# Kernel optimization log

Hardware: AMD Instinct MI355X
Metric: run time of the kernel (lower is better)

Reference implementation:

```python
import jax, jax.numpy as jnp
import numpy as np

B, L, D = 8, 2048, 1024
NH, M = 32, 16            # TTTConfig defaults: num_attention_heads=32, mini_batch_size=16
HD = D // NH              # 32
NM = L // M               # 128 mini-batches
DI = 2048                 # FFN hidden (configs.d_lower)
BASE_LR = 1.0
EPS = 1e-6


def setup_inputs() -> dict:
    key = jax.random.key(0)
    ks = jax.random.split(key, 12)
    n = lambda k, s, sc=0.02: jax.random.normal(k, s, jnp.float32) * sc
    return dict(
        enc_input=jax.random.normal(ks[0], (B, L, D), jnp.float32),
        ln0_g=jnp.ones((D,), jnp.float32), ln0_b=jnp.zeros((D,), jnp.float32),
        Wq=n(ks[1], (D, D)), Wk=n(ks[2], (D, D)), Wv=n(ks[3], (D, D)), Wo=n(ks[4], (D, D)),
        W1=n(ks[5], (NH, HD, HD)), b1=jnp.zeros((NH, 1, HD), jnp.float32),
        token_idx_delta=jnp.zeros((M,), jnp.float32),
        lr_w=n(ks[6], (NH, D)), lr_b=jnp.zeros((NH,), jnp.float32),
        ttt_ln_g=jnp.ones((NH, HD), jnp.float32), ttt_ln_b=jnp.zeros((NH, HD), jnp.float32),
        post_g=jnp.ones((D,), jnp.float32), post_b=jnp.zeros((D,), jnp.float32),
        ffn_g=jnp.ones((D,), jnp.float32), ffn_b=jnp.zeros((D,), jnp.float32),
        fw1=n(ks[7], (D, DI)), fb1=jnp.zeros((DI,), jnp.float32),
        fw2=n(ks[8], (DI, D)), fb2=jnp.zeros((D,), jnp.float32),
    )


def _layernorm(x, g, b):
    mu = x.mean(-1, keepdims=True)
    v = ((x - mu) ** 2).mean(-1, keepdims=True)
    return (x - mu) * jax.lax.rsqrt(v + EPS) * g + b


def _rope(x):
    # x: [B,NH,L,HD]; standard rotary embedding, theta=10000
    half = HD // 2
    inv = 1.0 / (10000.0 ** (jnp.arange(0, HD, 2, dtype=jnp.float32) / HD))
    pos = jnp.arange(L, dtype=jnp.float32)
    fr = pos[:, None] * inv[None, :]                    # [L, HD/2]
    emb = jnp.concatenate([fr, fr], -1)                 # [L, HD]
    cos, sin = jnp.cos(emb), jnp.sin(emb)
    rot = jnp.concatenate([-x[..., half:], x[..., :half]], -1)
    return x * cos + rot * sin


def reference(enc_input, ln0_g, ln0_b, Wq, Wk, Wv, Wo, W1, b1, token_idx_delta,
              lr_w, lr_b, ttt_ln_g, ttt_ln_b, post_g, post_b,
              ffn_g, ffn_b, fw1, fb1, fw2, fb2):
    residual = enc_input
    x = _layernorm(enc_input, ln0_g, ln0_b)

    def heads(t):  # [B,L,D] -> [B,NH,L,HD]
        return t.reshape(B, L, NH, HD).transpose(0, 2, 1, 3)

    XQ = _rope(heads(x @ Wq))
    XK = _rope(heads(x @ Wk))
    XV = heads(x @ Wv)

    # per-token learnable learning rates (sigmoid gate), token_idx schedule
    X_mb = x.reshape(B, NM, M, D)
    ttt_lr = jax.nn.sigmoid(jnp.einsum('bnkc,hc->bhnk', X_mb, lr_w) + lr_b[None, :, None, None])
    ttt_lr_eta = BASE_LR * ttt_lr / HD                               # [B,NH,NM,M]
    token_idx = jnp.clip(1.0 / jnp.arange(1, M + 1, dtype=jnp.float32) + token_idx_delta, 0.0, None)
    eta = token_idx[None, None, None, :, None] * ttt_lr_eta[:, :, :, None, :]  # [B,NH,NM,M,M]

    def to_scan(t):  # [B,NH,L,HD] -> [NM,B,NH,M,HD]
        return t.reshape(B, NH, NM, M, HD).transpose(2, 0, 1, 3, 4)

    xs = (to_scan(XQ), to_scan(XK), to_scan(XV), eta.transpose(2, 0, 1, 3, 4))

    lw = ttt_ln_g[:, None, :]   # [NH,1,HD]
    lb = ttt_ln_b[:, None, :]
    tril = jnp.tril(jnp.ones((M, M), jnp.float32))

    def ln_fwd(z):
        mu = z.mean(-1, keepdims=True)
        v = ((z - mu) ** 2).mean(-1, keepdims=True)
        return (z - mu) * jax.lax.rsqrt(v + EPS) * lw + lb

    def ln_l2_bwd(z, tgt):
        # gradient of 0.5*||LN(z)-tgt||^2 w.r.t. z (fused LN l2 backward)
        mu = z.mean(-1, keepdims=True)
        v = ((z - mu) ** 2).mean(-1, keepdims=True)
        std = jnp.sqrt(v + EPS)
        xhat = (z - mu) / std
        gxh = (xhat * lw + lb - tgt) * lw
        return (HD * gxh - gxh.sum(-1, keepdims=True)
                - xhat * (gxh * xhat).sum(-1, keepdims=True)) / (HD * std)

    W1_0 = jnp.broadcast_to(W1[None], (B, NH, HD, HD))
    b1_0 = jnp.broadcast_to(b1[None], (B, NH, 1, HD))

    def step(carry, inp):
        W, bvec = carry
        q, k, v_, e = inp                                    # [B,NH,M,HD], e: [B,NH,M,M]
        Z1 = k @ W + bvec
        grad = ln_l2_bwd(Z1, v_ - k)                         # [B,NH,M,HD]
        Attn1 = tril * (q @ k.transpose(0, 1, 3, 2))         # causal dual-form attention
        b_bar = bvec - (tril * e) @ grad
        Z1_bar = q @ W - (e * Attn1) @ grad + b_bar
        last_e = e[:, :, -1, :, None]                        # [B,NH,M,1]
        W_new = W - (last_e * k).transpose(0, 1, 3, 2) @ grad
        b_new = bvec - (last_e * grad).sum(-2, keepdims=True)
        return (W_new, b_new), q + ln_fwd(Z1_bar)

    _, outs = jax.lax.scan(step, (W1_0, b1_0), xs)           # [NM,B,NH,M,HD]
    out = outs.transpose(1, 0, 3, 2, 4).reshape(B, L, D)     # -> [B,L,D]
    out = _layernorm(out, post_g, post_b) @ Wo               # post_norm + o_proj
    out = out + residual                                     # dropout = identity (eval)

    # PositionWiseFeedForward (pre-LN, residual)
    r2 = out
    h = _layernorm(out, ffn_g, ffn_b)
    h = jax.nn.relu(h @ fw1 + fb1) @ fw2 + fb2
    return h + r2
```

## Files before the change

### kernel.cpp

```cpp
#include <hip/hip_runtime.h>
#include <hip/hip_bf16.h>
#include <stdint.h>

#define B_   8
#define L_   2048
#define D_   1024
#define NH_  32
#define M_   16
#define NM_  128
#define HD_  32
#define DI_  2048
#define BL_  16384
#define EPS_ 1e-6f

typedef __attribute__((ext_vector_type(8))) short  s16x8;
typedef __attribute__((ext_vector_type(4))) short  s16x4;
typedef __attribute__((ext_vector_type(8))) __bf16 bf16x8;
typedef __attribute__((ext_vector_type(4))) float  f32x4;
typedef __attribute__((ext_vector_type(4))) unsigned u32x4;
typedef __attribute__((ext_vector_type(2))) unsigned u32x2;

__device__ __forceinline__ float bf2f(short s){
  unsigned u = ((unsigned)(unsigned short)s) << 16;
  return __builtin_bit_cast(float, u);
}
__device__ __forceinline__ short f2bf(float f){
  unsigned u = __builtin_bit_cast(unsigned, f);
  u = u + 0x7FFFu + ((u >> 16) & 1u);
  return (short)(u >> 16);
}
__device__ __forceinline__ unsigned cvtpk(float lo, float hi){
  unsigned r;
  asm("v_cvt_pk_bf16_f32 %0, %1, %2" : "=v"(r) : "v"(lo), "v"(hi));
  return r;
}
__device__ __forceinline__ void mfma16x2(s16x4 a, s16x4 b0, s16x4 b1,
                                         f32x4& c0, f32x4& c1){
  asm volatile(
      "s_nop 1\n\t"
      "v_mfma_f32_16x16x16_bf16 %0, %2, %3, %0\n\t"
      "v_mfma_f32_16x16x16_bf16 %1, %2, %4, %1\n\t"
      "s_nop 7\n\t"
      "s_nop 3"
      : "+v"(c0), "+v"(c1) : "v"(a), "v"(b0), "v"(b1));
}
template<int N>
__device__ __forceinline__ float ror_add(float v){
  const int y = __builtin_amdgcn_update_dpp(
      0, __builtin_bit_cast(int, v), 0x120 + N, 0xF, 0xF, true);
  return v + __builtin_bit_cast(float, y);
}
__device__ __forceinline__ float rsum16d(float v){
  v = ror_add<1>(v); v = ror_add<2>(v); v = ror_add<4>(v); v = ror_add<8>(v);
  return v;
}
__device__ __forceinline__ void wgbar(){
  asm volatile("s_waitcnt lgkmcnt(0)" ::: "memory");
  __builtin_amdgcn_s_barrier();
  __builtin_amdgcn_sched_barrier(0);
}
__device__ __forceinline__ void gl16(const void* g, void* l){
  __builtin_amdgcn_global_load_lds(
      (const __attribute__((address_space(1))) void*)g,
      (__attribute__((address_space(3))) void*)l, 16, 0, 0);
}

__global__ __launch_bounds__(256) void transpose_cast(
    const float* __restrict__ in, short* __restrict__ out, int R, int Cc)
{
  __shared__ float t[32][33];
  const int lx = threadIdx.x & 31, ly = threadIdx.x >> 5;
  const int r0 = blockIdx.y * 32, c0 = blockIdx.x * 32;
  #pragma unroll
  for (int s = 0; s < 4; ++s){
    const int r = ly + s*8;
    t[r][lx] = in[(size_t)(r0 + r)*Cc + c0 + lx];
  }
  __syncthreads();
  #pragma unroll
  for (int s = 0; s < 4; ++s){
    const int r = ly + s*8;
    out[(size_t)(c0 + r)*R + r0 + lx] = f2bf(t[lx][r]);
  }
}

struct TC4 { const float *s0,*s1,*s2,*s3; short *d0,*d1,*d2,*d3; };
__global__ __launch_bounds__(256) void transpose_cast4(TC4 p)
{
  __shared__ float t[32][33];
  const int z = blockIdx.z;
  const float* in = (z==0)?p.s0:(z==1)?p.s1:(z==2)?p.s2:p.s3;
  short* out      = (z==0)?p.d0:(z==1)?p.d1:(z==2)?p.d2:p.d3;
  const int lx = threadIdx.x & 31, ly = threadIdx.x >> 5;
  const int r0 = blockIdx.y * 32, c0 = blockIdx.x * 32;
  #pragma unroll
  for (int s = 0; s < 4; ++s){
    const int r = ly + s*8;
    t[r][lx] = in[(size_t)(r0 + r)*1024 + c0 + lx];
  }
  __syncthreads();
  #pragma unroll
  for (int s = 0; s < 4; ++s){
    const int r = ly + s*8;
    out[(size_t)(c0 + r)*1024 + r0 + lx] = f2bf(t[lx][r]);
  }
}

__global__ __launch_bounds__(256) void misc_prep(
    const float* __restrict__ lr_w, short* __restrict__ lrwb,
    float* __restrict__ ct, float* __restrict__ st)
{
  const int idx = blockIdx.x*256 + threadIdx.x;
  if (idx < NH_*D_){
    lrwb[idx] = f2bf(lr_w[idx]);
  } else {
    const int k = idx - NH_*D_;
    const int l = k >> 4, j = k & 15;
    const float inv = powf(10000.f, -(float)j * (1.f/16.f));
    const float fr  = (float)l * inv;
    ct[k] = cosf(fr);
    st[k] = sinf(fr);
  }
}

__global__ __launch_bounds__(256) void ln_rows(
    const float* __restrict__ in, const float* __restrict__ g,
    const float* __restrict__ bta, short* __restrict__ out)
{
  const int row = blockIdx.x, tid = threadIdx.x;
  const float4 v = ((const float4*)(in + (size_t)row*D_))[tid];
  float s  = v.x + v.y + v.z + v.w;
  float s2 = v.x*v.x + v.y*v.y + v.z*v.z + v.w*v.w;
  #pragma unroll
  for (int m = 1; m < 64; m <<= 1){ s += __shfl_xor(s, m); s2 += __shfl_xor(s2, m); }
  __shared__ float rs[4], rq[4];
  if ((tid & 63) == 0){ rs[tid>>6] = s; rq[tid>>6] = s2; }
  __syncthreads();
  s  = rs[0] + rs[1] + rs[2] + rs[3];
  s2 = rq[0] + rq[1] + rq[2] + rq[3];
  const float mu   = s  * (1.f/D_);
  const float var  = s2 * (1.f/D_) - mu*mu;
  const float rstd = rsqrtf(var + EPS_);
  const float4 gg = ((const float4*)g)[tid];
  const float4 bb = ((const float4*)bta)[tid];
  s16x4 o;
  o[0] = f2bf((v.x - mu)*rstd*gg.x + bb.x);
  o[1] = f2bf((v.y - mu)*rstd*gg.y + bb.y);
  o[2] = f2bf((v.z - mu)*rstd*gg.z + bb.z);
  o[3] = f2bf((v.w - mu)*rstd*gg.w + bb.w);
  ((s16x4*)(out + (size_t)row*D_))[tid] = o;
}

__global__ __launch_bounds__(256) void ln_rows_bf(
    const short* __restrict__ in, const float* __restrict__ g,
    const float* __restrict__ bta, short* __restrict__ out)
{
  const int row = blockIdx.x, tid = threadIdx.x;
  const s16x4 v4 = ((const s16x4*)(in + (size_t)row*D_))[tid];
  float v[4];
  #pragma unroll
  for (int e = 0; e < 4; ++e) v[e] = bf2f(v4[e]);
  float s  = v[0]+v[1]+v[2]+v[3];
  float s2 = v[0]*v[0]+v[1]*v[1]+v[2]*v[2]+v[3]*v[3];
  #pragma unroll
  for (int m = 1; m < 64; m <<= 1){ s += __shfl_xor(s, m); s2 += __shfl_xor(s2, m); }
  __shared__ float rs[4], rq[4];
  if ((tid & 63) == 0){ rs[tid>>6] = s; rq[tid>>6] = s2; }
  __syncthreads();
  s  = rs[0] + rs[1] + rs[2] + rs[3];
  s2 = rq[0] + rq[1] + rq[2] + rq[3];
  const float mu   = s  * (1.f/D_);
  const float var  = s2 * (1.f/D_) - mu*mu;
  const float rstd = rsqrtf(var + EPS_);
  const float4 gg = ((const float4*)g)[tid];
  const float4 bb = ((const float4*)bta)[tid];
  s16x4 o;
  #pragma unroll
  for (int e = 0; e < 4; ++e){
    const float gv = (e==0)?gg.x:(e==1)?gg.y:(e==2)?gg.z:gg.w;
    const float bv = (e==0)?bb.x:(e==1)?bb.y:(e==2)?bb.z:bb.w;
    o[e] = f2bf((v[e] - mu)*rstd*gv + bv);
  }
  ((s16x4*)(out + (size_t)row*D_))[tid] = o;
}

template<int ACT, int OUTBF, int BIAS, int RES, int RESB, int QKVOUT>
__global__ __launch_bounds__(512, 2) void gemm256(
    const short* __restrict__ A, const short* __restrict__ Bt,
    const float* __restrict__ bias, const float* __restrict__ res,
    const short* __restrict__ resb,
    float* __restrict__ Cf, short* __restrict__ Cb,
    const float* __restrict__ ct, const float* __restrict__ st,
    int Mr, int N, int K)
{
  __shared__ __align__(16) short As[4][8192];
  __shared__ __align__(16) short Bs[4][8192];
  const int tid  = threadIdx.x;
  const int lane = tid & 63, wid = tid >> 6;
  const int wr = wid >> 2, wc = wid & 3;
  const int nwg = gridDim.x * gridDim.y;
  const int wg  = blockIdx.y * gridDim.x + blockIdx.x;
  const int swz = (wg & 7) * (nwg >> 3) + (wg >> 3);
  const int bx  = swz % gridDim.x, by = swz / gridDim.x;
  const int row0 = by * 256, col0 = bx * 256;

  f32x4 acc[8][4] = {};

  const int kswz = (((tid & 3) ^ ((tid >> 3) & 3)) << 3);
  const short* gAb = A  + (size_t)(row0 + (tid >> 2)) * K + kswz;
  const short* gBb = Bt + (size_t)(col0 + (tid >> 2)) * K + kswz;
  short* lAb = &As[0][0] + tid*8;
  short* lBb = &Bs[0][0] + tid*8;

  auto stage = [&](int bt2, int t2){
    const size_t kb = (size_t)t2 * 32;
    gl16(gAb + kb,                   lAb + bt2*8192);
    gl16(gAb + kb + 128*(size_t)K,   lAb + bt2*8192 + 4096);
    gl16(gBb + kb,                   lBb + bt2*8192);
    gl16(gBb + kb + 128*(size_t)K,   lBb + bt2*8192 + 4096);
  };

  const int fr = lane & 15;
  const int k0 = (((lane >> 4) ^ ((lane >> 1) & 3)) << 3);

  const int nK = K >> 5;
  stage(0, 0); stage(1, 1); stage(2, 2);
  asm volatile("s_waitcnt vmcnt(8)" ::: "memory");
  __builtin_amdgcn_s_barrier();

  for (int kt = 0; kt < nK; ++kt){
    const int bt = kt & 3;
    const short* Ab = &As[0][0] + bt*8192 + wr*4096;
    const short* Bb = &Bs[0][0] + bt*8192 + (wc >> 1)*4096 + (wc & 1)*2048;
    bf16x8 af[8], bfv[4];
    #pragma unroll
    for (int m = 0; m < 8; ++m)
      af[m] = *(const bf16x8*)(Ab + (m*16 + fr)*32 + k0);
    #pragma unroll
    for (int n = 0; n < 4; ++n)
      bfv[n] = *(const bf16x8*)(Bb + (n*16 + fr)*32 + k0);
    if (kt + 3 < nK) stage((kt + 3) & 3, kt + 3);
    __builtin_amdgcn_s_setprio(1);
    #pragma unroll
    for (int m = 0; m < 8; ++m)
      #pragma unroll
      for (int n = 0; n < 4; ++n)
        acc[m][n] = __builtin_amdgcn_mfma_f32_16x16x32_bf16(af[m], bfv[n], acc[m][n], 0,0,0);
    __builtin_amdgcn_s_setprio(0);
    if (kt + 3 < nK)      asm volatile("s_waitcnt vmcnt(8)" ::: "memory");
    else if (kt + 2 < nK) asm volatile("s_waitcnt vmcnt(4)" ::: "memory");
    else if (kt + 1 < nK) asm volatile("s_waitcnt vmcnt(0)" ::: "memory");
    __builtin_amdgcn_s_barrier();
  }

  const int cr = (lane >> 4) * 4, cc = lane & 15;
  if (QKVOUT){
    const int part = col0 >> 10;
    #pragma unroll
    for (int m = 0; m < 8; ++m){
      const int gr0 = row0 + wr*128 + m*16 + cr;
      const int bidx = gr0 >> 11, l0 = gr0 & (L_-1);
      const int nn = l0 >> 4;
      if (part < 2){
        #pragma unroll
        for (int np = 0; np < 2; ++np){
          const int gc = col0 + wc*64 + np*32 + cc;
          const int hh = (gc & 1023) >> 5;
          short* tile = Cb + ((size_t)(bidx*NH_ + hh)*NM_ + nn)*2048;
          s16x4 r0v, r1v;
          #pragma unroll
          for (int r = 0; r < 4; ++r){
            const int l = l0 + r;
            const float cv = ct[l*16 + cc], sv = st[l*16 + cc];
            const float x0 = acc[m][np*2][r], x1 = acc[m][np*2+1][r];
            const short q0 = f2bf(x0*cv - x1*sv);
            const short q1 = f2bf(x1*cv + x0*sv);
            tile[part*512 + (cr + r)*32 + cc]      = q0;
            tile[part*512 + (cr + r)*32 + cc + 16] = q1;
            r0v[r] = q0; r1v[r] = q1;
          }
          if (part == 1){
            *(s16x4*)(tile + 1024 + cc*16 + cr)      = r0v;
            *(s16x4*)(tile + 1024 + (cc+16)*16 + cr) = r1v;
          }
        }
      } else {
        #pragma unroll
        for (int n = 0; n < 4; ++n){
          const int gc = col0 + wc*64 + n*16 + cc;
          const int hh = (gc & 1023) >> 5, dd = gc & 31;
          short* tile = Cb + ((size_t)(bidx*NH_ + hh)*NM_ + nn)*2048;
          s16x4 p;
          #pragma unroll
          for (int r = 0; r < 4; ++r) p[r] = f2bf(acc[m][n][r]);
          *(s16x4*)(tile + 1536 + dd*16 + cr) = p;
        }
      }
    }
    return;
  }
  #pragma unroll
  for (int m = 0; m < 8; ++m){
    #pragma unroll
    for (int n = 0; n < 4; ++n){
      const int gc = col0 + wc*64 + n*16 + cc;
      float bv = 0.f;
      if (BIAS) bv = bias[gc];
      #pragma unroll
      for (int r = 0; r < 4; ++r){
        const int gr = row0 + wr*128 + m*16 + cr + r;
        float v = acc[m][n][r] + bv;
        if (RES)  v += res[(size_t)gr*N + gc];
        if (RESB) v += bf2f(resb[(size_t)gr*N + gc]);
        if (ACT == 1) v = fmaxf(v, 0.f);
        if (OUTBF) Cb[(size_t)gr*N + gc] = f2bf(v);
        else       Cf[(size_t)gr*N + gc] = v;
      }
    }
  }
}

__global__ __launch_bounds__(256) void eta_kernel(
    const short* __restrict__ xb, const short* __restrict__ lrwb,
    const float* __restrict__ lr_b, float* __restrict__ eta)
{
  __shared__ __align__(16) short wl[NH_*1032];
  const int tid = threadIdx.x;
  const int lane = tid & 63, wv = tid >> 6;
  const int li = lane & 15, lh = lane >> 4;
  #pragma unroll
  for (int s = 0; s < 16; ++s){
    const int e = tid + 256*s;
    const int hrow = e >> 7, c = (e & 127) * 8;
    *(s16x8*)(wl + hrow*1032 + c) = ((const s16x8*)lrwb)[e];
  }
  __syncthreads();

  const int t0 = (blockIdx.x*4 + wv) * 16;
  const short* xrow = xb + (size_t)(t0 + li)*1024 + 8*lh;
  const short* w0p = wl + li*1032 + 8*lh;
  const short* w1p = wl + (16 + li)*1032 + 8*lh;
  f32x4 acc0 = {}, acc1 = {};
  #pragma unroll 4
  for (int s = 0; s < 32; ++s){
    const bf16x8 a  = *(const bf16x8*)(xrow + s*32);
    const bf16x8 b0 = *(const bf16x8*)(w0p + s*32);
    const bf16x8 b1 = *(const bf16x8*)(w1p + s*32);
    acc0 = __builtin_amdgcn_mfma_f32_16x16x32_bf16(a, b0, acc0, 0,0,0);
    acc1 = __builtin_amdgcn_mfma_f32_16x16x32_bf16(a, b1, acc1, 0,0,0);
  }
  const int t = t0 + 4*lh;
  const int bidx = t >> 11, l = t & (L_-1), n = l >> 4, im = l & 15;
  float* e0 = eta + ((size_t)(bidx*NH_ + li)*NM_ + n)*M_ + im;
  float* e1 = eta + ((size_t)(bidx*NH_ + 16 + li)*NM_ + n)*M_ + im;
  const float lb0 = lr_b[li], lb1 = lr_b[16 + li];
  #pragma unroll
  for (int r = 0; r < 4; ++r){
    e0[r] = 1.f/(1.f + __expf(-(acc0[r] + lb0))) * (1.f/32.f);
    e1[r] = 1.f/(1.f + __expf(-(acc1[r] + lb1))) * (1.f/32.f);
  }
}

__global__ __launch_bounds__(192) void scan_kernel(
    const short* __restrict__ Q5, const float* __restrict__ eta,
    const float* __restrict__ W1, const float* __restrict__ b1,
    const float* __restrict__ tdelta, const float* __restrict__ lng,
    const float* __restrict__ lnb, short* __restrict__ out)
{
  const int bh = blockIdx.x;
  const int h = bh & 31, b = bh >> 5;
  const int lane = threadIdx.x & 63;
  const int wv = threadIdx.x >> 6;
  const int li = lane & 15, lh = lane >> 4;

  __shared__ __align__(16) short WTl[2][32*40];
  __shared__ __align__(16) unsigned PGl[2][256];
  __shared__ float BBl[2][2][16];
  __shared__ __align__(16) short QLl[2][16*40];

  const short* chain = Q5 + (size_t)bh * (NM_*2048);
  const float* ech   = eta + (size_t)bh * (NM_*16);

  float lw[2], lbv[2];
  #pragma unroll
  for (int hh = 0; hh < 2; ++hh){
    lw[hh]  = lng[h*32 + 16*hh + li];
    lbv[hh] = lnb[h*32 + 16*hh + li];
  }

  if (wv == 0){
    f32x4 Wq[2][2];
    #pragma unroll
    for (int rb = 0; rb < 2; ++rb)
      #pragma unroll
      for (int cb = 0; cb < 2; ++cb)
        #pragma unroll
        for (int r = 0; r < 4; ++r)
          Wq[rb][cb][r] = W1[h*1024 + (16*rb + 4*lh + r)*32 + 16*cb + li];
    float bb[2];
    bb[0] = b1[h*32 + li];  bb[1] = b1[h*32 + 16 + li];
    const float lef = fmaxf(1.f/16.f + tdelta[15], 0.f);

    auto writeWT = [&](int sl){
      #pragma unroll
      for (int cb = 0; cb < 2; ++cb)
        #pragma unroll
        for (int rb = 0; rb < 2; ++rb){
          const unsigned p0 = cvtpk(Wq[rb][cb][0], Wq[rb][cb][1]);
          const unsigned p1 = cvtpk(Wq[rb][cb][2], Wq[rb][cb][3]);
          *(uint64_t*)(&WTl[sl][0] + (16*cb + li)*40 + 16*rb + 4*lh) =
              ((uint64_t)p1 << 32) | p0;
        }
    };
    auto readWf = [&](int sl, bf16x8* Wf){
      Wf[0] = *(const bf16x8*)(&WTl[sl][0] + li*40 + 8*lh);
      Wf[1] = *(const bf16x8*)(&WTl[sl][0] + (16 + li)*40 + 8*lh);
    };

    writeWT(0);
    if (lh == 0){ BBl[0][0][li] = bb[0]; BBl[0][1][li] = bb[1]; }
    bf16x8 Wf[2];
    readWf(0, Wf);

    struct P0 { s16x8 kA; s16x4 kTe0, kTe1, vTe0, vTe1;
                f32x4 lr0, lr1, lr2, lr3; };
    auto ld0 = [&](int n) -> P0 {
      const short* t = chain + (size_t)n*2048;
      const float* e = ech + n*16;
      P0 p;
      p.kA   = *(const s16x8*)(t + 512 + li*32 + 8*lh);
      p.kTe0 = *(const s16x4*)(t + 1024 + li*16 + 4*lh);
      p.kTe1 = *(const s16x4*)(t + 1024 + (16 + li)*16 + 4*lh);
      p.vTe0 = *(const s16x4*)(t + 1536 + li*16 + 4*lh);
      p.vTe1 = *(const s16x4*)(t + 1536 + (16 + li)*16 + 4*lh);
      p.lr0 = *(const f32x4*)(e);     p.lr1 = *(const f32x4*)(e + 4);
      p.lr2 = *(const f32x4*)(e + 8); p.lr3 = *(const f32x4*)(e + 12);
      return p;
    };

    P0 cur = ld0(0);
    wgbar();

    #pragma unroll 1
    for (int p = 0; p <= NM_; ++p){
      if (p < NM_){
        const int n = p;
        const int sl = n & 1;
        P0 nxt = ld0(n + 1 < NM_ ? n + 1 : NM_ - 1);
        const bf16x8 kAf = __builtin_bit_cast(bf16x8, cur.kA);

        f32x4 zac[2];
        #pragma unroll
        for (int hh = 0; hh < 2; ++hh){
          f32x4 c0; c0[0]=bb[hh]; c0[1]=bb[hh]; c0[2]=bb[hh]; c0[3]=bb[hh];
          zac[hh] = __builtin_amdgcn_mfma_f32_16x16x32_bf16(kAf, Wf[hh], c0, 0,0,0);
        }

        float xh[2][4], grad[2][4], rstdv[4];
        #pragma unroll
        for (int r = 0; r < 4; ++r){
          float s  = rsum16d(zac[0][r] + zac[1][r]);
          float q2 = rsum16d(zac[0][r]*zac[0][r] + zac[1][r]*zac[1][r]);
          const float mu  = s * (1.f/32.f);
          const float var = q2 * (1.f/32.f) - mu*mu;
          const float rstd = rsqrtf(var + EPS_);
          rstdv[r] = rstd;
          xh[0][r] = (zac[0][r] - mu) * rstd;
          xh[1][r] = (zac[1][r] - mu) * rstd;
        }
        #pragma unroll
        for (int r = 0; r < 4; ++r){
          const float t0 = bf2f(cur.vTe0[r]) - bf2f(cur.kTe0[r]);
          const float t1 = bf2f(cur.vTe1[r]) - bf2f(cur.kTe1[r]);
          const float g0 = (xh[0][r]*lw[0] + lbv[0] - t0)*lw[0];
          const float g1 = (xh[1][r]*lw[1] + lbv[1] - t1)*lw[1];
          const float sg  = rsum16d(g0 + g1);
          const float sgx = rsum16d(g0*xh[0][r] + g1*xh[1][r]);
          const float f = rstdv[r] * (1.f/32.f);
          grad[0][r] = (32.f*g0 - sg - xh[0][r]*sgx) * f;
          grad[1][r] = (32.f*g1 - sg - xh[1][r]*sgx) * f;
        }

        const unsigned g00 = cvtpk(grad[0][0], grad[0][1]);
        const unsigned g01 = cvtpk(grad[0][2], grad[0][3]);
        const unsigned g10 = cvtpk(grad[1][0], grad[1][1]);
        const unsigned g11 = cvtpk(grad[1][2], grad[1][3]);
        u32x4 gq; gq[0]=g00; gq[1]=g01; gq[2]=g10; gq[3]=g11;
        *(u32x4*)&PGl[sl][lane*4] = gq;
        u32x2 tg0; tg0[0]=g00; tg0[1]=g01;
        u32x2 tg1; tg1[0]=g10; tg1[1]=g11;
        const s16x4 gB0 = __builtin_bit_cast(s16x4, tg0);
        const s16x4 gB1 = __builtin_bit_cast(s16x4, tg1);

        f32x4 lrq;
        { const f32x4 t0 = (lh & 1) ? cur.lr1 : cur.lr0;
          const f32x4 t1 = (lh & 1) ? cur.lr3 : cur.lr2;
          lrq = (lh & 2) ? t1 : t0; }

        #pragma unroll
        for (int rb = 0; rb < 2; ++rb){
          const s16x4 kq = rb ? cur.kTe1 : cur.kTe0;
          const unsigned a0 = cvtpk(-lef*lrq[0]*bf2f(kq[0]), -lef*lrq[1]*bf2f(kq[1]));
          const unsigned a1 = cvtpk(-lef*lrq[2]*bf2f(kq[2]), -lef*lrq[3]*bf2f(kq[3]));
          u32x2 ta; ta[0]=a0; ta[1]=a1;
          const s16x4 afq = __builtin_bit_cast(s16x4, ta);
          mfma16x2(afq, gB0, gB1, Wq[rb][0], Wq[rb][1]);
        }

        writeWT(sl ^ 1);
        readWf(sl ^ 1, Wf);

        #pragma unroll
        for (int hh = 0; hh < 2; ++hh){
          float t = 0.f;
          #pragma unroll
          for (int r = 0; r < 4; ++r) t += lrq[r]*grad[hh][r];
          t += __shfl_xor(t, 16); t += __shfl_xor(t, 32);
          bb[hh] -= lef * t;
        }
        if (lh == 0){ BBl[sl ^ 1][0][li] = bb[0]; BBl[sl ^ 1][1][li] = bb[1]; }
        cur = nxt;
      }
      wgbar();
    }
  } else {
    const int par = wv - 1;
    const float tok_i = fmaxf(1.f/(float)(li+1) + tdelta[li], 0.f);
    short* outp = out + (size_t)b*L_*D_ + h*32;

    struct P1 { s16x8 qA, kA; f32x4 lr0, lr1, lr2, lr3; };
    auto ld1 = [&](int n) -> P1 {
      const short* t = chain + (size_t)n*2048;
      const float* e = ech + n*16;
      P1 p;
      p.qA = *(const s16x8*)(t + li*32 + 8*lh);
      p.kA = *(const s16x8*)(t + 512 + li*32 + 8*lh);
      p.lr0 = *(const f32x4*)(e);     p.lr1 = *(const f32x4*)(e + 4);
      p.lr2 = *(const f32x4*)(e + 8); p.lr3 = *(const f32x4*)(e + 12);
      return p;
    };

    auto outln = [&](int n, const f32x4* yac){
      #pragma unroll
      for (int r = 0; r < 4; ++r){
        const float s  = rsum16d(yac[0][r] + yac[1][r]);
        const float q2 = rsum16d(yac[0][r]*yac[0][r] + yac[1][r]*yac[1][r]);
        const float mu   = s * (1.f/32.f);
        const float var  = q2 * (1.f/32.f) - mu*mu;
        const float rstd = rsqrtf(var + EPS_);
        const int row = 4*lh + r;
        #pragma unroll
        for (int hh = 0; hh < 2; ++hh){
          const float qv = bf2f(QLl[n & 1][row*40 + 16*hh + li]);
          const float o  = qv + (yac[hh][r] - mu)*rstd*lw[hh] + lbv[hh];
          outp[(size_t)(n*16 + row)*D_ + 16*hh + li] = f2bf(o);
        }
      }
    };

    P1 cur = ld1(par);
    wgbar();

    f32x4 ycur[2] = {};
    s16x4 pCur4 = {};
    #pragma unroll 1
    for (int p = 0; p <= NM_; ++p){
      if (p >= 1 && ((p - 1) & 1) == par){
        const int m = p - 1;
        const int sl = m & 1;
        const u32x4 gq = *(const u32x4*)&PGl[sl][lane*4];
        u32x2 tg0; tg0[0]=gq[0]; tg0[1]=gq[1];
        u32x2 tg1; tg1[0]=gq[2]; tg1[1]=gq[3];
        const s16x4 gB0 = __builtin_bit_cast(s16x4, tg0);
        const s16x4 gB1 = __builtin_bit_cast(s16x4, tg1);
        mfma16x2(pCur4, gB0, gB1, ycur[0], ycur[1]);
        outln(m, ycur);
      }
      if (p < NM_ && (p & 1) == par){
        const int sl = p & 1;
        bf16x8 Wf0 = *(const bf16x8*)(&WTl[sl][0] + li*40 + 8*lh);
        bf16x8 Wf1 = *(const bf16x8*)(&WTl[sl][0] + (16 + li)*40 + 8*lh);
        const float bb0 = BBl[sl][0][li];
        const float bb1 = BBl[sl][1][li];

        P1 nxt = ld1(p + 2 < NM_ ? p + 2 : p);
        const bf16x8 qAf = __builtin_bit_cast(bf16x8, cur.qA);
        const bf16x8 kAf = __builtin_bit_cast(bf16x8, cur.kA);

        *(s16x8*)(&QLl[sl][0] + li*40 + 8*lh) = cur.qA;

        f32x4 zz = {};
        const f32x4 aacT = __builtin_amdgcn_mfma_f32_16x16x32_bf16(kAf, qAf, zz, 0,0,0);

        f32x4 lrq;
        { const f32x4 t0 = (lh & 1) ? cur.lr1 : cur.lr0;
          const f32x4 t1 = (lh & 1) ? cur.lr3 : cur.lr2;
          lrq = (lh & 2) ? t1 : t0; }

        float pv[4];
        #pragma unroll
        for (int e = 0; e < 4; ++e){
          const bool ok = (4*lh + e <= li);
          pv[e] = ok ? -tok_i * lrq[e] * (1.f + aacT[e]) : 0.f;
        }
        u32x2 tp; tp[0] = cvtpk(pv[0], pv[1]); tp[1] = cvtpk(pv[2], pv[3]);
        pCur4 = __builtin_bit_cast(s16x4, tp);

        { f32x4 c0; c0[0]=bb0; c0[1]=bb0; c0[2]=bb0; c0[3]=bb0;
          ycur[0] = __builtin_amdgcn_mfma_f32_16x16x32_bf16(qAf, Wf0, c0, 0,0,0); }
        { f32x4 c0; c0[0]=bb1; c0[1]=bb1; c0[2]=bb1; c0[3]=bb1;
          ycur[1] = __builtin_amdgcn_mfma_f32_16x16x32_bf16(qAf, Wf1, c0, 0,0,0); }

        cur = nxt;
      }
      wgbar();
    }
  }
}

extern "C" void kernel_launch(void* const* d_in, const int* in_sizes, int n_in,
                              void* d_out, int out_size, void* d_ws, size_t ws_size,
                              hipStream_t stream)
{
  const float* enc    = (const float*)d_in[0];
  const float* ln0_g  = (const float*)d_in[1];
  const float* ln0_b  = (const float*)d_in[2];
  const float* Wq     = (const float*)d_in[3];
  const float* Wk     = (const float*)d_in[4];
  const float* Wv     = (const float*)d_in[5];
  const float* Wo     = (const float*)d_in[6];
  const float* W1     = (const float*)d_in[7];
  const float* b1     = (const float*)d_in[8];
  const float* tdelta = (const float*)d_in[9];
  const float* lr_w   = (const float*)d_in[10];
  const float* lr_b   = (const float*)d_in[11];
  const float* ttt_g  = (const float*)d_in[12];
  const float* ttt_b  = (const float*)d_in[13];
  const float* post_g = (const float*)d_in[14];
  const float* post_b = (const float*)d_in[15];
  const float* ffn_g  = (const float*)d_in[16];
  const float* ffn_b  = (const float*)d_in[17];
  const float* fw1    = (const float*)d_in[18];
  const float* fb1    = (const float*)d_in[19];
  const float* fw2    = (const float*)d_in[20];
  const float* fb2    = (const float*)d_in[21];

  char* ws = (char*)d_ws;
  short* Q5    = (short*)(ws + 0);
  short* XB    = (short*)(ws + 134217728);
  short* SCANB = (short*)(ws + 134217728);
  short* WQKVT = (short*)(ws + 167772160);
  short* WOT   = (short*)(ws + 174063616);
  short* FW1T  = (short*)(ws + 176160768);
  short* FW2T  = (short*)(ws + 180355072);
  short* LRWB  = (short*)(ws + 184549376);
  float* CT    = (float*)(ws + 184614912);
  float* ST    = (float*)(ws + 184745984);
  float* ETA   = (float*)(ws + 184877056);
  short* YB    = (short*)(ws + 0);
  short* HB    = (short*)(ws + 33554432);
  short* T1    = (short*)(ws + 67108864);
  short* R2B   = (short*)(ws + 134217728);
  float* R2    = (float*)d_out;

  dim3 b256(256), b512(512);
  TC4 tc;
  tc.s0 = Wq; tc.s1 = Wk; tc.s2 = Wv; tc.s3 = Wo;
  tc.d0 = WQKVT; tc.d1 = WQKVT + 1048576; tc.d2 = WQKVT + 2097152; tc.d3 = WOT;
  transpose_cast4<<<dim3(32,32,4), b256, 0, stream>>>(tc);
  transpose_cast<<<dim3(64,32), b256, 0, stream>>>(fw1, FW1T, D_, DI_);
  transpose_cast<<<dim3(32,64), b256, 0, stream>>>(fw2, FW2T, DI_, D_);
  misc_prep<<<dim3(256), b256, 0, stream>>>(lr_w, LRWB, CT, ST);

  ln_rows<<<BL_, b256, 0, stream>>>(enc, ln0_g, ln0_b, XB);
  gemm256<0,0,0,0,0,1><<<dim3(12,64), b512, 0, stream>>>(XB, WQKVT, nullptr, nullptr, nullptr,
                                                         nullptr, Q5, CT, ST, BL_, 3072, D_);
  eta_kernel<<<dim3(256), b256, 0, stream>>>(XB, LRWB, lr_b, ETA);
  scan_kernel<<<dim3(256), dim3(192), 0, stream>>>(Q5, ETA, W1, b1, tdelta,
                                                   ttt_g, ttt_b, SCANB);
  ln_rows_bf<<<BL_, b256, 0, stream>>>(SCANB, post_g, post_b, YB);
  gemm256<0,1,0,1,0,0><<<dim3(4,64), b512, 0, stream>>>(YB, WOT, nullptr, enc, nullptr,
                                                        nullptr, R2B, nullptr, nullptr, BL_, D_, D_);
  ln_rows_bf<<<BL_, b256, 0, stream>>>(R2B, ffn_g, ffn_b, HB);
  gemm256<1,1,1,0,0,0><<<dim3(8,64), b512, 0, stream>>>(HB, FW1T, fb1, nullptr, nullptr,
                                                        nullptr, T1, nullptr, nullptr, BL_, DI_, D_);
  gemm256<0,0,1,0,1,0><<<dim3(4,64), b512, 0, stream>>>(T1, FW2T, fb2, nullptr, R2B,
                                                        R2, nullptr, nullptr, nullptr, BL_, D_, DI_);
}
```

Measured before the change: 507.9 us.

## Process two mini-batches per barrier in scan and deepen LDS ring to eight slots

The producer wave now runs two sequential mini-batch updates per workgroup barrier, with a two-deep register prefetch of chain data. Shared buffers for W, gradients and bias grow from two to eight slots so it can run ahead. The two consumer waves each handle one mini-batch per superstep, lagging by one superstep. Each consumer now does its attention, gradient MFMA and output layernorm in one step instead of splitting them across barriers. The aim is to halve the barrier count on the serial recurrence, at the cost of more LDS and register pressure.

Measured after the change: 485.1 us (median of 2 runs). -4.5%, faster.

```diff
diff --git a/kernel.cpp b/kernel.cpp
--- a/kernel.cpp
+++ b/kernel.cpp
@@ -373,9 +373,9 @@
   const int wv = threadIdx.x >> 6;
   const int li = lane & 15, lh = lane >> 4;
 
-  __shared__ __align__(16) short WTl[2][32*40];
-  __shared__ __align__(16) unsigned PGl[2][256];
-  __shared__ float BBl[2][2][16];
+  __shared__ __align__(16) short WTl[8][32*40];
+  __shared__ __align__(16) unsigned PGl[8][256];
+  __shared__ float BBl[8][2][16];
   __shared__ __align__(16) short QLl[2][16*40];
 
   const short* chain = Q5 + (size_t)bh * (NM_*2048);
@@ -439,87 +439,92 @@
     };
 
     P0 cur = ld0(0);
+    P0 nxt = ld0(1);
     wgbar();
 
     #pragma unroll 1
-    for (int p = 0; p <= NM_; ++p){
-      if (p < NM_){
-        const int n = p;
-        const int sl = n & 1;
-        P0 nxt = ld0(n + 1 < NM_ ? n + 1 : NM_ - 1);
-        const bf16x8 kAf = __builtin_bit_cast(bf16x8, cur.kA);
-
-        f32x4 zac[2];
+    for (int p = 0; p <= 64; ++p){
+      if (p < 64){
         #pragma unroll
-        for (int hh = 0; hh < 2; ++hh){
-          f32x4 c0; c0[0]=bb[hh]; c0[1]=bb[hh]; c0[2]=bb[hh]; c0[3]=bb[hh];
-          zac[hh] = __builtin_amdgcn_mfma_f32_16x16x32_bf16(kAf, Wf[hh], c0, 0,0,0);
+        for (int s = 0; s < 2; ++s){
+          const int n = 2*p + s;
+          P0 pf = ld0(n + 2 < NM_ ? n + 2 : NM_ - 1);
+          const bf16x8 kAf = __builtin_bit_cast(bf16x8, cur.kA);
+
+          f32x4 zac[2];
+          #pragma unroll
+          for (int hh = 0; hh < 2; ++hh){
+            f32x4 c0; c0[0]=bb[hh]; c0[1]=bb[hh]; c0[2]=bb[hh]; c0[3]=bb[hh];
+            zac[hh] = __builtin_amdgcn_mfma_f32_16x16x32_bf16(kAf, Wf[hh], c0, 0,0,0);
+          }
+
+          float xh[2][4], grad[2][4], rstdv[4];
+          #pragma unroll
+          for (int r = 0; r < 4; ++r){
+            float ss = rsum16d(zac[0][r] + zac[1][r]);
+            float q2 = rsum16d(zac[0][r]*zac[0][r] + zac[1][r]*zac[1][r]);
+            const float mu  = ss * (1.f/32.f);
+            const float var = q2 * (1.f/32.f) - mu*mu;
+            const float rstd = rsqrtf(var + EPS_);
+            rstdv[r] = rstd;
+            xh[0][r] = (zac[0][r] - mu) * rstd;
+            xh[1][r] = (zac[1][r] - mu) * rstd;
+          }
+          #pragma unroll
+          for (int r = 0; r < 4; ++r){
+            const float t0 = bf2f(cur.vTe0[r]) - bf2f(cur.kTe0[r]);
+            const float t1 = bf2f(cur.vTe1[r]) - bf2f(cur.kTe1[r]);
+            const float g0 = (xh[0][r]*lw[0] + lbv[0] - t0)*lw[0];
+            const float g1 = (xh[1][r]*lw[1] + lbv[1] - t1)*lw[1];
+            const float sg  = rsum16d(g0 + g1);
+            const float sgx = rsum16d(g0*xh[0][r] + g1*xh[1][r]);
+            const float f = rstdv[r] * (1.f/32.f);
+            grad[0][r] = (32.f*g0 - sg - xh[0][r]*sgx) * f;
+            grad[1][r] = (32.f*g1 - sg - xh[1][r]*sgx) * f;
+          }
+
+          f32x4 lrq;
+          { const f32x4 t0 = (lh & 1) ? cur.lr1 : cur.lr0;
+            const f32x4 t1 = (lh & 1) ? cur.lr3 : cur.lr2;
+            lrq = (lh & 2) ? t1 : t0; }
+
+          float tb0 = 0.f, tb1 = 0.f;
+          #pragma unroll
+          for (int r = 0; r < 4; ++r){ tb0 += lrq[r]*grad[0][r]; tb1 += lrq[r]*grad[1][r]; }
+          tb0 += __shfl_xor(tb0, 16); tb1 += __shfl_xor(tb1, 16);
+          tb0 += __shfl_xor(tb0, 32); tb1 += __shfl_xor(tb1, 32);
+
+          const unsigned g00 = cvtpk(grad[0][0], grad[0][1]);
+          const unsigned g01 = cvtpk(grad[0][2], grad[0][3]);
+          const unsigned g10 = cvtpk(grad[1][0], grad[1][1]);
+          const unsigned g11 = cvtpk(grad[1][2], grad[1][3]);
+          u32x4 gq; gq[0]=g00; gq[1]=g01; gq[2]=g10; gq[3]=g11;
+          *(u32x4*)&PGl[n & 7][lane*4] = gq;
+          u32x2 tg0; tg0[0]=g00; tg0[1]=g01;
+          u32x2 tg1; tg1[0]=g10; tg1[1]=g11;
+          const s16x4 gB0 = __builtin_bit_cast(s16x4, tg0);
+          const s16x4 gB1 = __builtin_bit_cast(s16x4, tg1);
+
+          #pragma unroll
+          for (int rb = 0; rb < 2; ++rb){
+            const s16x4 kq = rb ? cur.kTe1 : cur.kTe0;
+            const unsigned a0 = cvtpk(-lef*lrq[0]*bf2f(kq[0]), -lef*lrq[1]*bf2f(kq[1]));
+            const unsigned a1 = cvtpk(-lef*lrq[2]*bf2f(kq[2]), -lef*lrq[3]*bf2f(kq[3]));
+            u32x2 ta; ta[0]=a0; ta[1]=a1;
+            const s16x4 afq = __builtin_bit_cast(s16x4, ta);
+            mfma16x2(afq, gB0, gB1, Wq[rb][0], Wq[rb][1]);
+          }
+
+          bb[0] -= lef * tb0;
+          bb[1] -= lef * tb1;
+
+          const int so = (n + 1) & 7;
+          writeWT(so);
+          readWf(so, Wf);
+          if (lh == 0){ BBl[so][0][li] = bb[0]; BBl[so][1][li] = bb[1]; }
+          cur = nxt;
+          nxt = pf;
         }
-
-        float xh[2][4], grad[2][4], rstdv[4];
-        #pragma unroll
-        for (int r = 0; r < 4; ++r){
-          float s  = rsum16d(zac[0][r] + zac[1][r]);
-          float q2 = rsum16d(zac[0][r]*zac[0][r] + zac[1][r]*zac[1][r]);
-          const float mu  = s * (1.f/32.f);
-          const float var = q2 * (1.f/32.f) - mu*mu;
-          const float rstd = rsqrtf(var + EPS_);
-          rstdv[r] = rstd;
-          xh[0][r] = (zac[0][r] - mu) * rstd;
-          xh[1][r] = (zac[1][r] - mu) * rstd;
-        }
-        #pragma unroll
-        for (int r = 0; r < 4; ++r){
-          const float t0 = bf2f(cur.vTe0[r]) - bf2f(cur.kTe0[r]);
-          const float t1 = bf2f(cur.vTe1[r]) - bf2f(cur.kTe1[r]);
-          const float g0 = (xh[0][r]*lw[0] + lbv[0] - t0)*lw[0];
-          const float g1 = (xh[1][r]*lw[1] + lbv[1] - t1)*lw[1];
-          const float sg  = rsum16d(g0 + g1);
-          const float sgx = rsum16d(g0*xh[0][r] + g1*xh[1][r]);
-          const float f = rstdv[r] * (1.f/32.f);
-          grad[0][r] = (32.f*g0 - sg - xh[0][r]*sgx) * f;
-          grad[1][r] = (32.f*g1 - sg - xh[1][r]*sgx) * f;
-        }
-
-        const unsigned g00 = cvtpk(grad[0][0], grad[0][1]);
-        const unsigned g01 = cvtpk(grad[0][2], grad[0][3]);
-        const unsigned g10 = cvtpk(grad[1][0], grad[1][1]);
-        const unsigned g11 = cvtpk(grad[1][2], grad[1][3]);
-        u32x4 gq; gq[0]=g00; gq[1]=g01; gq[2]=g10; gq[3]=g11;
-        *(u32x4*)&PGl[sl][lane*4] = gq;
-        u32x2 tg0; tg0[0]=g00; tg0[1]=g01;
-        u32x2 tg1; tg1[0]=g10; tg1[1]=g11;
-        const s16x4 gB0 = __builtin_bit_cast(s16x4, tg0);
-        const s16x4 gB1 = __builtin_bit_cast(s16x4, tg1);
-
-        f32x4 lrq;
-        { const f32x4 t0 = (lh & 1) ? cur.lr1 : cur.lr0;
-          const f32x4 t1 = (lh & 1) ? cur.lr3 : cur.lr2;
-          lrq = (lh & 2) ? t1 : t0; }
-
-        #pragma unroll
-        for (int rb = 0; rb < 2; ++rb){
-          const s16x4 kq = rb ? cur.kTe1 : cur.kTe0;
-          const unsigned a0 = cvtpk(-lef*lrq[0]*bf2f(kq[0]), -lef*lrq[1]*bf2f(kq[1]));
-          const unsigned a1 = cvtpk(-lef*lrq[2]*bf2f(kq[2]), -lef*lrq[3]*bf2f(kq[3]));
-          u32x2 ta; ta[0]=a0; ta[1]=a1;
-          const s16x4 afq = __builtin_bit_cast(s16x4, ta);
-          mfma16x2(afq, gB0, gB1, Wq[rb][0], Wq[rb][1]);
-        }
-
-        writeWT(sl ^ 1);
-        readWf(sl ^ 1, Wf);
-
-        #pragma unroll
-        for (int hh = 0; hh < 2; ++hh){
-          float t = 0.f;
-          #pragma unroll
-          for (int r = 0; r < 4; ++r) t += lrq[r]*grad[hh][r];
-          t += __shfl_xor(t, 16); t += __shfl_xor(t, 32);
-          bb[hh] -= lef * t;
-        }
-        if (lh == 0){ BBl[sl ^ 1][0][li] = bb[0]; BBl[sl ^ 1][1][li] = bb[1]; }
-        cur = nxt;
       }
       wgbar();
     }
@@ -540,54 +545,25 @@
       return p;
     };
 
-    auto outln = [&](int n, const f32x4* yac){
-      #pragma unroll
-      for (int r = 0; r < 4; ++r){
-        const float s  = rsum16d(yac[0][r] + yac[1][r]);
-        const float q2 = rsum16d(yac[0][r]*yac[0][r] + yac[1][r]*yac[1][r]);
-        const float mu   = s * (1.f/32.f);
-        const float var  = q2 * (1.f/32.f) - mu*mu;
-        const float rstd = rsqrtf(var + EPS_);
-        const int row = 4*lh + r;
-        #pragma unroll
-        for (int hh = 0; hh < 2; ++hh){
-          const float qv = bf2f(QLl[n & 1][row*40 + 16*hh + li]);
-          const float o  = qv + (yac[hh][r] - mu)*rstd*lw[hh] + lbv[hh];
-          outp[(size_t)(n*16 + row)*D_ + 16*hh + li] = f2bf(o);
-        }
-      }
-    };
-
     P1 cur = ld1(par);
     wgbar();
 
-    f32x4 ycur[2] = {};
-    s16x4 pCur4 = {};
     #pragma unroll 1
-    for (int p = 0; p <= NM_; ++p){
-      if (p >= 1 && ((p - 1) & 1) == par){
-        const int m = p - 1;
-        const int sl = m & 1;
-        const u32x4 gq = *(const u32x4*)&PGl[sl][lane*4];
-        u32x2 tg0; tg0[0]=gq[0]; tg0[1]=gq[1];
-        u32x2 tg1; tg1[0]=gq[2]; tg1[1]=gq[3];
-        const s16x4 gB0 = __builtin_bit_cast(s16x4, tg0);
-        const s16x4 gB1 = __builtin_bit_cast(s16x4, tg1);
-        mfma16x2(pCur4, gB0, gB1, ycur[0], ycur[1]);
-        outln(m, ycur);
-      }
-      if (p < NM_ && (p & 1) == par){
-        const int sl = p & 1;
+    for (int p = 1; p <= 65; ++p){
+      if (p >= 2){
+        const int n = 2*(p - 2) + par;
+        const int sl = n & 7;
+        P1 pf = ld1(n + 2 < NM_ ? n + 2 : NM_ - 1);
+
         bf16x8 Wf0 = *(const bf16x8*)(&WTl[sl][0] + li*40 + 8*lh);
         bf16x8 Wf1 = *(const bf16x8*)(&WTl[sl][0] + (16 + li)*40 + 8*lh);
         const float bb0 = BBl[sl][0][li];
         const float bb1 = BBl[sl][1][li];
 
-        P1 nxt = ld1(p + 2 < NM_ ? p + 2 : p);
         const bf16x8 qAf = __builtin_bit_cast(bf16x8, cur.qA);
         const bf16x8 kAf = __builtin_bit_cast(bf16x8, cur.kA);
 
-        *(s16x8*)(&QLl[sl][0] + li*40 + 8*lh) = cur.qA;
+        *(s16x8*)(&QLl[par][0] + li*40 + 8*lh) = cur.qA;
 
         f32x4 zz = {};
         const f32x4 aacT = __builtin_amdgcn_mfma_f32_16x16x32_bf16(kAf, qAf, zz, 0,0,0);
@@ -604,14 +580,37 @@
           pv[e] = ok ? -tok_i * lrq[e] * (1.f + aacT[e]) : 0.f;
         }
         u32x2 tp; tp[0] = cvtpk(pv[0], pv[1]); tp[1] = cvtpk(pv[2], pv[3]);
-        pCur4 = __builtin_bit_cast(s16x4, tp);
-
+        const s16x4 pA4 = __builtin_bit_cast(s16x4, tp);
+
+        f32x4 yac[2];
         { f32x4 c0; c0[0]=bb0; c0[1]=bb0; c0[2]=bb0; c0[3]=bb0;
-          ycur[0] = __builtin_amdgcn_mfma_f32_16x16x32_bf16(qAf, Wf0, c0, 0,0,0); }
+          yac[0] = __builtin_amdgcn_mfma_f32_16x16x32_bf16(qAf, Wf0, c0, 0,0,0); }
         { f32x4 c0; c0[0]=bb1; c0[1]=bb1; c0[2]=bb1; c0[3]=bb1;
-          ycur[1] = __builtin_amdgcn_mfma_f32_16x16x32_bf16(qAf, Wf1, c0, 0,0,0); }
-
-        cur = nxt;
+          yac[1] = __builtin_amdgcn_mfma_f32_16x16x32_bf16(qAf, Wf1, c0, 0,0,0); }
+
+        const u32x4 gq = *(const u32x4*)&PGl[sl][lane*4];
+        u32x2 tg0; tg0[0]=gq[0]; tg0[1]=gq[1];
+        u32x2 tg1; tg1[0]=gq[2]; tg1[1]=gq[3];
+        const s16x4 gB0 = __builtin_bit_cast(s16x4, tg0);
+        const s16x4 gB1 = __builtin_bit_cast(s16x4, tg1);
+        mfma16x2(pA4, gB0, gB1, yac[0], yac[1]);
+
+        #pragma unroll
+        for (int r = 0; r < 4; ++r){
+          const float ss = rsum16d(yac[0][r] + yac[1][r]);
+          const float q2 = rsum16d(yac[0][r]*yac[0][r] + yac[1][r]*yac[1][r]);
+          const float mu   = ss * (1.f/32.f);
+          const float var  = q2 * (1.f/32.f) - mu*mu;
+          const float rstd = rsqrtf(var + EPS_);
+          const int row = 4*lh + r;
+          #pragma unroll
+          for (int hh = 0; hh < 2; ++hh){
+            const float qv = bf2f(QLl[par][row*40 + 16*hh + li]);
+            const float o  = qv + (yac[hh][r] - mu)*rstd*lw[hh] + lbv[hh];
+            outp[(size_t)(n*16 + row)*D_ + 16*hh + li] = f2bf(o);
+          }
+        }
+        cur = pf;
       }
       wgbar();
     }
```
